# Kernel optimization log

Measured on AMD Instinct MI355X. Metric: run time of the kernel, lower is better.

## Reference

```python
import jax, jax.numpy as jnp
import numpy as np

B, IN, H, L, S = 256, 256, 256, 2, 128


def setup_inputs() -> dict:
    key = jax.random.key(0)
    ks = jax.random.split(key, 13)
    inp = {
        "x": jax.random.normal(ks[0], (B, IN), jnp.float32),
        "hidden_stack": jax.random.normal(ks[1], (S + 1, B, H, L), jnp.float32) * 0.1,
        "cell_stack": jax.random.normal(ks[2], (S + 1, B, H, L), jnp.float32) * 0.1,
        "w_ih0": jax.random.normal(ks[3], (4 * H, IN), jnp.float32) / np.sqrt(IN).astype(np.float32),
        "w_hh0": jax.random.normal(ks[4], (4 * H, H), jnp.float32) / np.sqrt(H).astype(np.float32),
        "b_ih0": jax.random.normal(ks[5], (4 * H,), jnp.float32) * 0.01,
        "b_hh0": jax.random.normal(ks[6], (4 * H,), jnp.float32) * 0.01,
        "w_ih1": jax.random.normal(ks[7], (4 * H, H), jnp.float32) / np.sqrt(H).astype(np.float32),
        "w_hh1": jax.random.normal(ks[8], (4 * H, H), jnp.float32) / np.sqrt(H).astype(np.float32),
        "b_ih1": jax.random.normal(ks[9], (4 * H,), jnp.float32) * 0.01,
        "b_hh1": jax.random.normal(ks[10], (4 * H,), jnp.float32) * 0.01,
        "op": jax.random.randint(ks[11], (B,), 0, 3, jnp.int32) - 1,  # {-1,0,1}: pop/hold/push
        "pos": jax.random.randint(ks[12], (B,), 1, S, jnp.int32),      # in-bounds for pos+1 and pos+op
    }
    return inp


def _lstm_cell(x, h, c, w_ih, w_hh, b_ih, b_hh):
    # torch.nn.LSTMCell gate order: input, forget, cell(g), output
    g = x @ w_ih.T + h @ w_hh.T + b_ih + b_hh  # (B, 4H)
    i, f, gg, o = jnp.split(g, 4, axis=-1)
    c2 = jax.nn.sigmoid(f) * c + jax.nn.sigmoid(i) * jnp.tanh(gg)
    h2 = jax.nn.sigmoid(o) * jnp.tanh(c2)
    return h2, c2


def reference(x, hidden_stack, cell_stack, w_ih0, w_hh0, b_ih0, b_hh0,
              w_ih1, w_hh1, b_ih1, b_hh1, op, pos):
    bidx = jnp.arange(x.shape[0])
    # gather current top-of-stack state: (B, H, L)
    cur_h = hidden_stack[pos, bidx]
    cur_c = cell_stack[pos, bidx]
    # two-layer LSTM cell (layer 1 feeds on layer 0 hidden)
    h0, c0 = _lstm_cell(x, cur_h[..., 0], cur_c[..., 0], w_ih0, w_hh0, b_ih0, b_hh0)
    h1, c1 = _lstm_cell(h0, cur_h[..., 1], cur_c[..., 1], w_ih1, w_hh1, b_ih1, b_hh1)
    next_h = jnp.stack([h0, h1], axis=-1)  # (B, H, L)
    next_c = jnp.stack([c0, c1], axis=-1)
    # scatter new state at pos+1
    hidden_stack = hidden_stack.at[pos + 1, bidx].set(next_h)
    cell_stack = cell_stack.at[pos + 1, bidx].set(next_c)
    # move stack pointer, gather return state
    new_pos = pos + op
    ret_h = hidden_stack[new_pos, bidx]  # (B, H, L)
    ret_c = cell_stack[new_pos, bidx]
    # faithful to torch source: hidden_ret[:, :, -1] -> shape (1, B, L)
    h_out = ret_h[:, -1, :][None]
    c_out = ret_c[:, -1, :][None]
    return h_out, c_out, hidden_stack, cell_stack
```

## Files before the change

### kernel.cpp

```cpp
#include <hip/hip_runtime.h>


static __device__ __forceinline__ float sigf(float x) {
    return 1.0f / (1.0f + __expf(-x));
}
static __device__ __forceinline__ float tanh_fast(float x) {
    return 2.0f / (1.0f + __expf(-2.0f * x)) - 1.0f;
}

#define GBM 16
#define GBN 64
#define GBK 32

__global__ __launch_bounds__(256) void gemm_k(
    const float* __restrict__ a_lo,
    const float* __restrict__ a_hi,
    const int*   __restrict__ pos,
    const float* __restrict__ wih,
    const float* __restrict__ whh,
    const float* __restrict__ bih,
    const float* __restrict__ bhh,
    float* __restrict__ gates)
{
    __shared__ float As[GBK][GBM + 1];
    __shared__ float Ws[GBK][GBN + 4];
    int t   = threadIdx.x;
    int bm0 = (blockIdx.x >> 4) * GBM;
    int jt0 = (blockIdx.x & 15) * GBN;
    int arow = t >> 4;
    int akk  = (t & 15) * 2;
    int wrow = t >> 2;
    int wkb  = (t & 3) * 8;
    int tx = t & 15, ty = t >> 4;
    int ab = bm0 + arow;
    int ap = pos[ab];
    int wj = jt0 + wrow;

    float2 apre;
    float4 wpre0, wpre1;
    {
        int k = akk;
        apre = *(const float2*)&a_lo[ab * 256 + k];
        const float* ws = &wih[wj * 256 + wkb];
        wpre0 = *(const float4*)ws;
        wpre1 = *(const float4*)(ws + 4);
    }
    float acc[4] = {0.f, 0.f, 0.f, 0.f};
    for (int kt = 0; kt < 512; kt += GBK) {
        __syncthreads();
        As[akk][arow]     = apre.x;
        As[akk + 1][arow] = apre.y;
        Ws[wkb][wrow]     = wpre0.x;
        Ws[wkb + 1][wrow] = wpre0.y;
        Ws[wkb + 2][wrow] = wpre0.z;
        Ws[wkb + 3][wrow] = wpre0.w;
        Ws[wkb + 4][wrow] = wpre1.x;
        Ws[wkb + 5][wrow] = wpre1.y;
        Ws[wkb + 6][wrow] = wpre1.z;
        Ws[wkb + 7][wrow] = wpre1.w;
        int kt2 = kt + GBK;
        if (kt2 < 512) {
            int k = kt2 + akk;
            if (k < 256) {
                apre = *(const float2*)&a_lo[ab * 256 + k];
            } else {
                const float* ah = a_hi + ((ap * 256 + ab) * 256 + (k - 256)) * 2;
                apre.x = ah[0];
                apre.y = ah[2];
            }
            int kk = kt2 + wkb;
            const float* ws = (kk < 256) ? &wih[wj * 256 + kk]
                                         : &whh[wj * 256 + kk - 256];
            wpre0 = *(const float4*)ws;
            wpre1 = *(const float4*)(ws + 4);
        }
        __syncthreads();
        #pragma unroll
        for (int k = 0; k < GBK; ++k) {
            float a   = As[k][ty];
            float4 bv = *(const float4*)&Ws[k][tx * 4];
            acc[0] = fmaf(a, bv.x, acc[0]);
            acc[1] = fmaf(a, bv.y, acc[1]);
            acc[2] = fmaf(a, bv.z, acc[2]);
            acc[3] = fmaf(a, bv.w, acc[3]);
        }
    }
    int j = jt0 + tx * 4;
    float4 b0 = *(const float4*)&bih[j];
    float4 b1 = *(const float4*)&bhh[j];
    float4 r;
    r.x = acc[0] + b0.x + b1.x;
    r.y = acc[1] + b0.y + b1.y;
    r.z = acc[2] + b0.z + b1.z;
    r.w = acc[3] + b0.w + b1.w;
    *(float4*)&gates[(bm0 + ty) * 1024 + j] = r;
}

__global__ __launch_bounds__(256) void act0_k(
    const float* __restrict__ gates,
    const float* __restrict__ cel,
    const int*   __restrict__ pos,
    float* __restrict__ h0f, float* __restrict__ c0f)
{
    int e = blockIdx.x * 256 + threadIdx.x;
    int b = e >> 8, h = e & 255;
    float cin = cel[((pos[b] * 256 + b) * 256 + h) * 2];
    const float* g = gates + b * 1024 + h;
    float gi = g[0], gf = g[256], gg = g[512], go = g[768];
    float c  = sigf(gf) * cin + sigf(gi) * tanh_fast(gg);
    h0f[e] = sigf(go) * tanh_fast(c);
    c0f[e] = c;
}

#define NV4_PER_STACK 4227072
#define NCOPY_BLOCKS  33024
#define STACK_ELEMS   16908288

static __device__ __forceinline__ void lstm1(
    const float* __restrict__ gates, const float* __restrict__ cel,
    int p, int b, int h, float& hv, float& cv)
{
    float cin = cel[((p * 256 + b) * 256 + h) * 2 + 1];
    const float* g = gates + b * 1024 + h;
    float gi = g[0], gf = g[256], gg = g[512], go = g[768];
    cv = sigf(gf) * cin + sigf(gi) * tanh_fast(gg);
    hv = sigf(go) * tanh_fast(cv);
}

__global__ __launch_bounds__(256) void copy_k(
    const float* __restrict__ hid, const float* __restrict__ cel,
    const int* __restrict__ pos, const int* __restrict__ op,
    const float* __restrict__ h0f, const float* __restrict__ c0f,
    const float* __restrict__ gates,
    float* __restrict__ out)
{
    if (blockIdx.x == NCOPY_BLOCKS) {
        int b = threadIdx.x;
        int o = op[b];
        int p = pos[b];
        float h0v, h1v, c0v, c1v;
        if (o == 1) {
            h0v = h0f[b * 256 + 255];
            c0v = c0f[b * 256 + 255];
            lstm1(gates, cel, p, b, 255, h1v, c1v);
        } else {
            int base2 = (((p + o) * 256 + b) * 256 + 255) * 2;
            h0v = hid[base2]; h1v = hid[base2 + 1];
            c0v = cel[base2]; c1v = cel[base2 + 1];
        }
        out[b * 2]           = h0v;
        out[b * 2 + 1]       = h1v;
        out[512 + b * 2]     = c0v;
        out[512 + b * 2 + 1] = c1v;
        return;
    }
    int v = blockIdx.x * 256 + threadIdx.x;
    bool is_cell = v >= NV4_PER_STACK;
    int vv = is_cell ? v - NV4_PER_STACK : v;
    int s   = vv >> 15;
    int rem = vv & 32767;
    int b   = rem >> 7;
    int q   = rem & 127;
    int p   = pos[b];
    float4 val;
    if (s == p + 1) {
        int h = q * 2;
        float h1a, c1a, h1b, c1b;
        lstm1(gates, cel, p, b, h,     h1a, c1a);
        lstm1(gates, cel, p, b, h + 1, h1b, c1b);
        if (is_cell) {
            val.x = c0f[b * 256 + h];     val.y = c1a;
            val.z = c0f[b * 256 + h + 1]; val.w = c1b;
        } else {
            val.x = h0f[b * 256 + h];     val.y = h1a;
            val.z = h0f[b * 256 + h + 1]; val.w = h1b;
        }
    } else {
        const float4* src = (const float4*)(is_cell ? cel : hid);
        val = src[vv];
    }
    float4* dst = (float4*)(out + 1024 + (is_cell ? STACK_ELEMS : 0));
    dst[vv] = val;
}

extern "C" void kernel_launch(void* const* d_in, const int* in_sizes, int n_in,
                              void* d_out, int out_size, void* d_ws, size_t ws_size,
                              hipStream_t stream) {
    const float* x    = (const float*)d_in[0];
    const float* hid  = (const float*)d_in[1];
    const float* cel  = (const float*)d_in[2];
    const float* wih0 = (const float*)d_in[3];
    const float* whh0 = (const float*)d_in[4];
    const float* bih0 = (const float*)d_in[5];
    const float* bhh0 = (const float*)d_in[6];
    const float* wih1 = (const float*)d_in[7];
    const float* whh1 = (const float*)d_in[8];
    const float* bih1 = (const float*)d_in[9];
    const float* bhh1 = (const float*)d_in[10];
    const int* op  = (const int*)d_in[11];
    const int* pos = (const int*)d_in[12];
    float* out = (float*)d_out;

    float* W    = (float*)d_ws;
    float* gates= W;
    float* h0f  = W + 262144;
    float* c0f  = W + 327680;

    gemm_k<<<256, 256, 0, stream>>>(x,   hid,     pos, wih0, whh0, bih0, bhh0, gates);
    act0_k<<<256, 256, 0, stream>>>(gates, cel, pos, h0f, c0f);
    gemm_k<<<256, 256, 0, stream>>>(h0f, hid + 1, pos, wih1, whh1, bih1, bhh1, gates);
    copy_k<<<NCOPY_BLOCKS + 1, 256, 0, stream>>>(
        hid, cel, pos, op, h0f, c0f, gates, out);
}
```

Baseline: 288.0 us.

## Overlap bulk stack copy with GEMM/activation kernels and scatter updated slot separately

```diff
diff --git a/kernel.cpp b/kernel.cpp
--- a/kernel.cpp
+++ b/kernel.cpp
@@ -12,7 +12,19 @@
 #define GBN 64
 #define GBK 32
 
-__global__ __launch_bounds__(256) void gemm_k(
+#define NV4_PER_STACK 4227072
+#define STACK_ELEMS   16908288
+#define CEL_CHUNK1    655360
+
+static __device__ __forceinline__ void copy_span(
+    int cb0, const float4* __restrict__ csrc, float4* __restrict__ cdst, int cn4)
+{
+    int stride = (gridDim.x - cb0) * 256;
+    for (int i = (blockIdx.x - cb0) * 256 + threadIdx.x; i < cn4; i += stride)
+        cdst[i] = csrc[i];
+}
+
+__global__ __launch_bounds__(256) void gemm_copy_k(
     const float* __restrict__ a_lo,
     const float* __restrict__ a_hi,
     const int*   __restrict__ pos,
@@ -20,8 +32,15 @@
     const float* __restrict__ whh,
     const float* __restrict__ bih,
     const float* __restrict__ bhh,
-    float* __restrict__ gates)
-{
+    float* __restrict__ gates,
+    const float4* __restrict__ csrc,
+    float4* __restrict__ cdst,
+    int cn4)
+{
+    if (blockIdx.x >= 256) {
+        copy_span(256, csrc, cdst, cn4);
+        return;
+    }
     __shared__ float As[GBK][GBM + 1];
     __shared__ float Ws[GBK][GBN + 4];
     int t   = threadIdx.x;
@@ -96,12 +115,19 @@
     *(float4*)&gates[(bm0 + ty) * 1024 + j] = r;
 }
 
-__global__ __launch_bounds__(256) void act0_k(
+__global__ __launch_bounds__(256) void act0_copy_k(
     const float* __restrict__ gates,
     const float* __restrict__ cel,
     const int*   __restrict__ pos,
-    float* __restrict__ h0f, float* __restrict__ c0f)
-{
+    float* __restrict__ h0f, float* __restrict__ c0f,
+    const float4* __restrict__ csrc,
+    float4* __restrict__ cdst,
+    int cn4)
+{
+    if (blockIdx.x >= 256) {
+        copy_span(256, csrc, cdst, cn4);
+        return;
+    }
     int e = blockIdx.x * 256 + threadIdx.x;
     int b = e >> 8, h = e & 255;
     float cin = cel[((pos[b] * 256 + b) * 256 + h) * 2];
@@ -112,10 +138,6 @@
     c0f[e] = c;
 }
 
-#define NV4_PER_STACK 4227072
-#define NCOPY_BLOCKS  33024
-#define STACK_ELEMS   16908288
-
 static __device__ __forceinline__ void lstm1(
     const float* __restrict__ gates, const float* __restrict__ cel,
     int p, int b, int h, float& hv, float& cv)
@@ -127,14 +149,14 @@
     hv = sigf(go) * tanh_fast(cv);
 }
 
-__global__ __launch_bounds__(256) void copy_k(
+__global__ __launch_bounds__(256) void slot_k(
     const float* __restrict__ hid, const float* __restrict__ cel,
     const int* __restrict__ pos, const int* __restrict__ op,
     const float* __restrict__ h0f, const float* __restrict__ c0f,
     const float* __restrict__ gates,
     float* __restrict__ out)
 {
-    if (blockIdx.x == NCOPY_BLOCKS) {
+    if (blockIdx.x == 256) {
         int b = threadIdx.x;
         int o = op[b];
         int p = pos[b];
@@ -155,32 +177,25 @@
         return;
     }
     int v = blockIdx.x * 256 + threadIdx.x;
-    bool is_cell = v >= NV4_PER_STACK;
-    int vv = is_cell ? v - NV4_PER_STACK : v;
-    int s   = vv >> 15;
-    int rem = vv & 32767;
-    int b   = rem >> 7;
-    int q   = rem & 127;
-    int p   = pos[b];
+    bool is_cell = v >= 32768;
+    int vv = v & 32767;
+    int b = vv >> 7;
+    int q = vv & 127;
+    int p = pos[b];
+    int h = q * 2;
+    float h1a, c1a, h1b, c1b;
+    lstm1(gates, cel, p, b, h,     h1a, c1a);
+    lstm1(gates, cel, p, b, h + 1, h1b, c1b);
     float4 val;
-    if (s == p + 1) {
-        int h = q * 2;
-        float h1a, c1a, h1b, c1b;
-        lstm1(gates, cel, p, b, h,     h1a, c1a);
-        lstm1(gates, cel, p, b, h + 1, h1b, c1b);
-        if (is_cell) {
-            val.x = c0f[b * 256 + h];     val.y = c1a;
-            val.z = c0f[b * 256 + h + 1]; val.w = c1b;
-        } else {
-            val.x = h0f[b * 256 + h];     val.y = h1a;
-            val.z = h0f[b * 256 + h + 1]; val.w = h1b;
-        }
+    if (is_cell) {
+        val.x = c0f[b * 256 + h];     val.y = c1a;
+        val.z = c0f[b * 256 + h + 1]; val.w = c1b;
     } else {
-        const float4* src = (const float4*)(is_cell ? cel : hid);
-        val = src[vv];
+        val.x = h0f[b * 256 + h];     val.y = h1a;
+        val.z = h0f[b * 256 + h + 1]; val.w = h1b;
     }
     float4* dst = (float4*)(out + 1024 + (is_cell ? STACK_ELEMS : 0));
-    dst[vv] = val;
+    dst[(p + 1) * 32768 + b * 128 + q] = val;
 }
 
 extern "C" void kernel_launch(void* const* d_in, const int* in_sizes, int n_in,
@@ -201,14 +216,26 @@
     const int* pos = (const int*)d_in[12];
     float* out = (float*)d_out;
 
-    float* W    = (float*)d_ws;
-    float* gates= W;
-    float* h0f  = W + 262144;
-    float* c0f  = W + 327680;
-
-    gemm_k<<<256, 256, 0, stream>>>(x,   hid,     pos, wih0, whh0, bih0, bhh0, gates);
-    act0_k<<<256, 256, 0, stream>>>(gates, cel, pos, h0f, c0f);
-    gemm_k<<<256, 256, 0, stream>>>(h0f, hid + 1, pos, wih1, whh1, bih1, bhh1, gates);
-    copy_k<<<NCOPY_BLOCKS + 1, 256, 0, stream>>>(
+    float* W     = (float*)d_ws;
+    float* gates = W;
+    float* h0f   = W + 262144;
+    float* c0f   = W + 327680;
+
+    float4*       hid_out = (float4*)(out + 1024);
+    float4*       cel_out = (float4*)(out + 1024 + STACK_ELEMS);
+    const float4* hid_in  = (const float4*)hid;
+    const float4* cel_in  = (const float4*)cel;
+
+    gemm_copy_k<<<256 + 2048, 256, 0, stream>>>(
+        x, hid, pos, wih0, whh0, bih0, bhh0, gates,
+        hid_in, hid_out, NV4_PER_STACK);
+    act0_copy_k<<<256 + 1024, 256, 0, stream>>>(
+        gates, cel, pos, h0f, c0f,
+        cel_in, cel_out, CEL_CHUNK1);
+    gemm_copy_k<<<256 + 2048, 256, 0, stream>>>(
+        h0f, hid + 1, pos, wih1, whh1, bih1, bhh1, gates,
+        cel_in + CEL_CHUNK1, cel_out + CEL_CHUNK1,
+        NV4_PER_STACK - CEL_CHUNK1);
+    slot_k<<<257, 256, 0, stream>>>(
         hid, cel, pos, op, h0f, c0f, gates, out);
 }
```

Result: faster. 266.7 us (-7.4%).

## Fuse LSTM steps into persistent kernel overlapping stack copy with GEMMs

Applied to the files above, without the earlier changes.

```diff
diff --git a/kernel.cpp b/kernel.cpp
--- a/kernel.cpp
+++ b/kernel.cpp
@@ -1,5 +1,11 @@
 #include <hip/hip_runtime.h>
 
+
+#define NV4   4227072
+#define CTOT  8454144
+#define S1T   2818048
+#define S2T   5636096
+#define STACK_ELEMS 16908288
 
 static __device__ __forceinline__ float sigf(float x) {
     return 1.0f / (1.0f + __expf(-x));
@@ -8,113 +14,153 @@
     return 2.0f / (1.0f + __expf(-2.0f * x)) - 1.0f;
 }
 
-#define GBM 16
-#define GBN 64
-#define GBK 32
-
-__global__ __launch_bounds__(256) void gemm_k(
-    const float* __restrict__ a_lo,
-    const float* __restrict__ a_hi,
-    const int*   __restrict__ pos,
-    const float* __restrict__ wih,
-    const float* __restrict__ whh,
-    const float* __restrict__ bih,
-    const float* __restrict__ bhh,
+static __device__ __forceinline__ void gbar(int* bar, int slot, int nb)
+{
+    __syncthreads();
+    if (threadIdx.x == 0) {
+        __threadfence();
+        int* arr = bar + slot * 2;
+        if (atomicAdd(arr, 1) == nb - 1) {
+            __hip_atomic_store(arr + 1, 1, __ATOMIC_RELEASE,
+                               __HIP_MEMORY_SCOPE_AGENT);
+        } else {
+            int spins = 0;
+            while (!__hip_atomic_load(arr + 1, __ATOMIC_ACQUIRE,
+                                      __HIP_MEMORY_SCOPE_AGENT)) {
+                __builtin_amdgcn_s_sleep(2);
+                if (++spins > (1 << 22)) break;
+            }
+        }
+        __threadfence();
+    }
+    __syncthreads();
+}
+
+static __device__ __forceinline__ void do_copy(
+    const float4* __restrict__ hin, float4* __restrict__ hout,
+    const float4* __restrict__ cin, float4* __restrict__ cout,
+    int lo, int hi, int cb, int ncb)
+{
+    int stride = ncb << 8;
+    int i = lo + (cb << 8) + (int)threadIdx.x;
+    int lim3 = hi - 3 * stride;
+    for (; i < lim3; i += stride << 2) {
+        int i1 = i + stride, i2 = i + 2 * stride, i3 = i + 3 * stride;
+        const float4* p0 = (i  < NV4) ? hin + i  : cin + (i  - NV4);
+        const float4* p1 = (i1 < NV4) ? hin + i1 : cin + (i1 - NV4);
+        const float4* p2 = (i2 < NV4) ? hin + i2 : cin + (i2 - NV4);
+        const float4* p3 = (i3 < NV4) ? hin + i3 : cin + (i3 - NV4);
+        float4 v0 = *p0, v1 = *p1, v2 = *p2, v3 = *p3;
+        float4* q0 = (i  < NV4) ? hout + i  : cout + (i  - NV4);
+        float4* q1 = (i1 < NV4) ? hout + i1 : cout + (i1 - NV4);
+        float4* q2 = (i2 < NV4) ? hout + i2 : cout + (i2 - NV4);
+        float4* q3 = (i3 < NV4) ? hout + i3 : cout + (i3 - NV4);
+        *q0 = v0; *q1 = v1; *q2 = v2; *q3 = v3;
+    }
+    for (; i < hi; i += stride) {
+        const float4* p = (i < NV4) ? hin + i : cin + (i - NV4);
+        float4 v = *p;
+        float4* q = (i < NV4) ? hout + i : cout + (i - NV4);
+        *q = v;
+    }
+}
+
+static __device__ __forceinline__ void gemm_block(
+    const float* __restrict__ a_lo, const float* __restrict__ a_hi,
+    const int* __restrict__ pos,
+    const float* __restrict__ wih, const float* __restrict__ whh,
+    const float* __restrict__ bih, const float* __restrict__ bhh,
     float* __restrict__ gates)
 {
-    __shared__ float As[GBK][GBM + 1];
-    __shared__ float Ws[GBK][GBN + 4];
+    __shared__ float As[32][36];
+    __shared__ float Ws[32][132];
     int t   = threadIdx.x;
-    int bm0 = (blockIdx.x >> 4) * GBM;
-    int jt0 = (blockIdx.x & 15) * GBN;
-    int arow = t >> 4;
-    int akk  = (t & 15) * 2;
-    int wrow = t >> 2;
-    int wkb  = (t & 3) * 8;
-    int tx = t & 15, ty = t >> 4;
-    int ab = bm0 + arow;
-    int ap = pos[ab];
+    int tb  = blockIdx.x;
+    int bm0 = (tb >> 3) << 5;
+    int jt0 = (tb & 7) << 7;
+    int arow = t >> 3, ak4 = (t & 7) << 2;
+    int ab = bm0 + arow, ap = pos[ab];
+    int wrow = t >> 1, wk = (t & 1) << 4;
     int wj = jt0 + wrow;
-
-    float2 apre;
-    float4 wpre0, wpre1;
+    int tx = t & 31, ty = t >> 5;
+
+    float4 apre, wpre0, wpre1, wpre2, wpre3;
+    apre = *(const float4*)&a_lo[ab * 256 + ak4];
     {
-        int k = akk;
-        apre = *(const float2*)&a_lo[ab * 256 + k];
-        const float* ws = &wih[wj * 256 + wkb];
-        wpre0 = *(const float4*)ws;
+        const float* ws = &wih[wj * 256 + wk];
+        wpre0 = *(const float4*)(ws + 0);
         wpre1 = *(const float4*)(ws + 4);
-    }
-    float acc[4] = {0.f, 0.f, 0.f, 0.f};
-    for (int kt = 0; kt < 512; kt += GBK) {
+        wpre2 = *(const float4*)(ws + 8);
+        wpre3 = *(const float4*)(ws + 12);
+    }
+    float acc[4][4] = {{0.f, 0.f, 0.f, 0.f}};
+    for (int s = 0; s < 16; ++s) {
         __syncthreads();
-        As[akk][arow]     = apre.x;
-        As[akk + 1][arow] = apre.y;
-        Ws[wkb][wrow]     = wpre0.x;
-        Ws[wkb + 1][wrow] = wpre0.y;
-        Ws[wkb + 2][wrow] = wpre0.z;
-        Ws[wkb + 3][wrow] = wpre0.w;
-        Ws[wkb + 4][wrow] = wpre1.x;
-        Ws[wkb + 5][wrow] = wpre1.y;
-        Ws[wkb + 6][wrow] = wpre1.z;
-        Ws[wkb + 7][wrow] = wpre1.w;
-        int kt2 = kt + GBK;
-        if (kt2 < 512) {
-            int k = kt2 + akk;
-            if (k < 256) {
-                apre = *(const float2*)&a_lo[ab * 256 + k];
+        As[ak4 + 0][arow] = apre.x;
+        As[ak4 + 1][arow] = apre.y;
+        As[ak4 + 2][arow] = apre.z;
+        As[ak4 + 3][arow] = apre.w;
+        Ws[wk + 0][wrow]  = wpre0.x;  Ws[wk + 1][wrow]  = wpre0.y;
+        Ws[wk + 2][wrow]  = wpre0.z;  Ws[wk + 3][wrow]  = wpre0.w;
+        Ws[wk + 4][wrow]  = wpre1.x;  Ws[wk + 5][wrow]  = wpre1.y;
+        Ws[wk + 6][wrow]  = wpre1.z;  Ws[wk + 7][wrow]  = wpre1.w;
+        Ws[wk + 8][wrow]  = wpre2.x;  Ws[wk + 9][wrow]  = wpre2.y;
+        Ws[wk + 10][wrow] = wpre2.z;  Ws[wk + 11][wrow] = wpre2.w;
+        Ws[wk + 12][wrow] = wpre3.x;  Ws[wk + 13][wrow] = wpre3.y;
+        Ws[wk + 14][wrow] = wpre3.z;  Ws[wk + 15][wrow] = wpre3.w;
+        if (s < 15) {
+            int kg = ((s + 1) << 5) + ak4;
+            if (kg < 256) {
+                apre = *(const float4*)&a_lo[ab * 256 + kg];
             } else {
-                const float* ah = a_hi + ((ap * 256 + ab) * 256 + (k - 256)) * 2;
-                apre.x = ah[0];
-                apre.y = ah[2];
+                const float* ah = a_hi + ((ap * 256 + ab) * 256 + (kg - 256)) * 2;
+                apre.x = ah[0]; apre.y = ah[2]; apre.z = ah[4]; apre.w = ah[6];
             }
-            int kk = kt2 + wkb;
+            int kk = ((s + 1) << 5) + wk;
             const float* ws = (kk < 256) ? &wih[wj * 256 + kk]
                                          : &whh[wj * 256 + kk - 256];
-            wpre0 = *(const float4*)ws;
+            wpre0 = *(const float4*)(ws + 0);
             wpre1 = *(const float4*)(ws + 4);
+            wpre2 = *(const float4*)(ws + 8);
+            wpre3 = *(const float4*)(ws + 12);
         }
         __syncthreads();
         #pragma unroll
-        for (int k = 0; k < GBK; ++k) {
-            float a   = As[k][ty];
-            float4 bv = *(const float4*)&Ws[k][tx * 4];
-            acc[0] = fmaf(a, bv.x, acc[0]);
-            acc[1] = fmaf(a, bv.y, acc[1]);
-            acc[2] = fmaf(a, bv.z, acc[2]);
-            acc[3] = fmaf(a, bv.w, acc[3]);
-        }
-    }
-    int j = jt0 + tx * 4;
+        for (int k = 0; k < 32; ++k) {
+            float4 av = *(const float4*)&As[k][ty << 2];
+            float4 wv = *(const float4*)&Ws[k][tx << 2];
+            acc[0][0] = fmaf(av.x, wv.x, acc[0][0]);
+            acc[0][1] = fmaf(av.x, wv.y, acc[0][1]);
+            acc[0][2] = fmaf(av.x, wv.z, acc[0][2]);
+            acc[0][3] = fmaf(av.x, wv.w, acc[0][3]);
+            acc[1][0] = fmaf(av.y, wv.x, acc[1][0]);
+            acc[1][1] = fmaf(av.y, wv.y, acc[1][1]);
+            acc[1][2] = fmaf(av.y, wv.z, acc[1][2]);
+            acc[1][3] = fmaf(av.y, wv.w, acc[1][3]);
+            acc[2][0] = fmaf(av.z, wv.x, acc[2][0]);
+            acc[2][1] = fmaf(av.z, wv.y, acc[2][1]);
+            acc[2][2] = fmaf(av.z, wv.z, acc[2][2]);
+            acc[2][3] = fmaf(av.z, wv.w, acc[2][3]);
+            acc[3][0] = fmaf(av.w, wv.x, acc[3][0]);
+            acc[3][1] = fmaf(av.w, wv.y, acc[3][1]);
+            acc[3][2] = fmaf(av.w, wv.z, acc[3][2]);
+            acc[3][3] = fmaf(av.w, wv.w, acc[3][3]);
+        }
+    }
+    int j = jt0 + (tx << 2);
     float4 b0 = *(const float4*)&bih[j];
     float4 b1 = *(const float4*)&bhh[j];
-    float4 r;
-    r.x = acc[0] + b0.x + b1.x;
-    r.y = acc[1] + b0.y + b1.y;
-    r.z = acc[2] + b0.z + b1.z;
-    r.w = acc[3] + b0.w + b1.w;
-    *(float4*)&gates[(bm0 + ty) * 1024 + j] = r;
-}
-
-__global__ __launch_bounds__(256) void act0_k(
-    const float* __restrict__ gates,
-    const float* __restrict__ cel,
-    const int*   __restrict__ pos,
-    float* __restrict__ h0f, float* __restrict__ c0f)
-{
-    int e = blockIdx.x * 256 + threadIdx.x;
-    int b = e >> 8, h = e & 255;
-    float cin = cel[((pos[b] * 256 + b) * 256 + h) * 2];
-    const float* g = gates + b * 1024 + h;
-    float gi = g[0], gf = g[256], gg = g[512], go = g[768];
-    float c  = sigf(gf) * cin + sigf(gi) * tanh_fast(gg);
-    h0f[e] = sigf(go) * tanh_fast(c);
-    c0f[e] = c;
-}
-
-#define NV4_PER_STACK 4227072
-#define NCOPY_BLOCKS  33024
-#define STACK_ELEMS   16908288
+    float* gp = gates + (bm0 + (ty << 2)) * 1024 + j;
+    #pragma unroll
+    for (int i = 0; i < 4; ++i) {
+        float4 r;
+        r.x = acc[i][0] + b0.x + b1.x;
+        r.y = acc[i][1] + b0.y + b1.y;
+        r.z = acc[i][2] + b0.z + b1.z;
+        r.w = acc[i][3] + b0.w + b1.w;
+        *(float4*)&gp[i * 1024] = r;
+    }
+}
 
 static __device__ __forceinline__ void lstm1(
     const float* __restrict__ gates, const float* __restrict__ cel,
@@ -127,14 +173,73 @@
     hv = sigf(go) * tanh_fast(cv);
 }
 
-__global__ __launch_bounds__(256) void copy_k(
-    const float* __restrict__ hid, const float* __restrict__ cel,
-    const int* __restrict__ pos, const int* __restrict__ op,
-    const float* __restrict__ h0f, const float* __restrict__ c0f,
-    const float* __restrict__ gates,
-    float* __restrict__ out)
-{
-    if (blockIdx.x == NCOPY_BLOCKS) {
+__global__ void init_k(int* bar) {
+    if (threadIdx.x < 8) bar[threadIdx.x] = 0;
+}
+
+__global__ __launch_bounds__(256, 4) void fused_k(
+    const float* __restrict__ x, const float* __restrict__ hid,
+    const float* __restrict__ cel,
+    const float* __restrict__ wih0, const float* __restrict__ whh0,
+    const float* __restrict__ bih0, const float* __restrict__ bhh0,
+    const float* __restrict__ wih1, const float* __restrict__ whh1,
+    const float* __restrict__ bih1, const float* __restrict__ bhh1,
+    const int* __restrict__ op, const int* __restrict__ pos,
+    float* __restrict__ gates, float* __restrict__ h0f,
+    float* __restrict__ c0f, float* __restrict__ out, int* bar)
+{
+    int bid = blockIdx.x, G = gridDim.x;
+    const float4* hin = (const float4*)hid;
+    const float4* cin = (const float4*)cel;
+    float4* hout = (float4*)(out + 1024);
+    float4* cout = (float4*)(out + 1024 + STACK_ELEMS);
+
+    if (bid < 64) gemm_block(x, hid, pos, wih0, whh0, bih0, bhh0, gates);
+    else          do_copy(hin, hout, cin, cout, 0, S1T, bid - 64, G - 64);
+    gbar(bar, 0, G);
+
+    if (bid < 64) {
+        #pragma unroll
+        for (int r = 0; r < 4; ++r) {
+            int e = r * 16384 + bid * 256 + (int)threadIdx.x;
+            int b = e >> 8, h = e & 255;
+            float cv0 = cel[((pos[b] * 256 + b) * 256 + h) * 2];
+            const float* g = gates + b * 1024 + h;
+            float gi = g[0], gf = g[256], gg = g[512], go = g[768];
+            float c  = sigf(gf) * cv0 + sigf(gi) * tanh_fast(gg);
+            h0f[e] = sigf(go) * tanh_fast(c);
+            c0f[e] = c;
+        }
+    } else {
+        do_copy(hin, hout, cin, cout, S1T, S2T, bid - 64, G - 64);
+    }
+    gbar(bar, 1, G);
+
+    if (bid < 64) gemm_block(h0f, hid + 1, pos, wih1, whh1, bih1, bhh1, gates);
+    else          do_copy(hin, hout, cin, cout, S2T, CTOT, bid - 64, G - 64);
+    gbar(bar, 2, G);
+
+    for (int v = bid * 256 + (int)threadIdx.x; v < 65536; v += G * 256) {
+        bool is_cell = v >= 32768;
+        int vv = v & 32767;
+        int b = vv >> 7, q = vv & 127;
+        int p = pos[b];
+        int h = q * 2;
+        float h1a, c1a, h1b, c1b;
+        lstm1(gates, cel, p, b, h,     h1a, c1a);
+        lstm1(gates, cel, p, b, h + 1, h1b, c1b);
+        float4 val;
+        if (is_cell) {
+            val.x = c0f[b * 256 + h];     val.y = c1a;
+            val.z = c0f[b * 256 + h + 1]; val.w = c1b;
+        } else {
+            val.x = h0f[b * 256 + h];     val.y = h1a;
+            val.z = h0f[b * 256 + h + 1]; val.w = h1b;
+        }
+        float4* dst = is_cell ? cout : hout;
+        dst[(p + 1) * 32768 + b * 128 + q] = val;
+    }
+    if (bid == 0) {
         int b = threadIdx.x;
         int o = op[b];
         int p = pos[b];
@@ -152,35 +257,7 @@
         out[b * 2 + 1]       = h1v;
         out[512 + b * 2]     = c0v;
         out[512 + b * 2 + 1] = c1v;
-        return;
-    }
-    int v = blockIdx.x * 256 + threadIdx.x;
-    bool is_cell = v >= NV4_PER_STACK;
-    int vv = is_cell ? v - NV4_PER_STACK : v;
-    int s   = vv >> 15;
-    int rem = vv & 32767;
-    int b   = rem >> 7;
-    int q   = rem & 127;
-    int p   = pos[b];
-    float4 val;
-    if (s == p + 1) {
-        int h = q * 2;
-        float h1a, c1a, h1b, c1b;
-        lstm1(gates, cel, p, b, h,     h1a, c1a);
-        lstm1(gates, cel, p, b, h + 1, h1b, c1b);
-        if (is_cell) {
-            val.x = c0f[b * 256 + h];     val.y = c1a;
-            val.z = c0f[b * 256 + h + 1]; val.w = c1b;
-        } else {
-            val.x = h0f[b * 256 + h];     val.y = h1a;
-            val.z = h0f[b * 256 + h + 1]; val.w = h1b;
-        }
-    } else {
-        const float4* src = (const float4*)(is_cell ? cel : hid);
-        val = src[vv];
-    }
-    float4* dst = (float4*)(out + 1024 + (is_cell ? STACK_ELEMS : 0));
-    dst[vv] = val;
+    }
 }
 
 extern "C" void kernel_launch(void* const* d_in, const int* in_sizes, int n_in,
@@ -201,14 +278,24 @@
     const int* pos = (const int*)d_in[12];
     float* out = (float*)d_out;
 
-    float* W    = (float*)d_ws;
-    float* gates= W;
-    float* h0f  = W + 262144;
-    float* c0f  = W + 327680;
-
-    gemm_k<<<256, 256, 0, stream>>>(x,   hid,     pos, wih0, whh0, bih0, bhh0, gates);
-    act0_k<<<256, 256, 0, stream>>>(gates, cel, pos, h0f, c0f);
-    gemm_k<<<256, 256, 0, stream>>>(h0f, hid + 1, pos, wih1, whh1, bih1, bhh1, gates);
-    copy_k<<<NCOPY_BLOCKS + 1, 256, 0, stream>>>(
-        hid, cel, pos, op, h0f, c0f, gates, out);
-}
+    float* W     = (float*)d_ws;
+    float* gates = W;
+    float* h0f   = W + 262144;
+    float* c0f   = W + 327680;
+    int*   bar   = (int*)(W + 393216);
+
+    static int G = 0;
+    if (G == 0) {
+        int maxb = 0;
+        if (hipOccupancyMaxActiveBlocksPerMultiprocessor(&maxb, fused_k, 256, 0)
+                != hipSuccess || maxb < 1)
+            maxb = 1;
+        G = maxb * 256;
+        if (G > 1024) G = 1024;
+    }
+
+    init_k<<<1, 64, 0, stream>>>(bar);
+    fused_k<<<G, 256, 0, stream>>>(x, hid, cel, wih0, whh0, bih0, bhh0,
+                                   wih1, whh1, bih1, bhh1, op, pos,
+                                   gates, h0f, c0f, out, bar);
+}
```

Result: slower. 501.6 us (+74.2%).
